# Kernel optimization log

Hardware: AMD Instinct MI355X
Metric: run time of the kernel (lower is better)

The kernel has to match this reference:

```python
import jax, jax.numpy as jnp
import numpy as np

TAU = 2.0      # spikingjelly LIFNode default tau
V_TH = 1.0     # default v_threshold
ALPHA = 4.0    # default surrogate.Sigmoid alpha


@jax.custom_vjp
def spike_fn(v):
    # Heaviside(v - v_th) with sigmoid surrogate gradient
    return (v >= V_TH).astype(v.dtype)

def _spike_fwd(v):
    return (v >= V_TH).astype(v.dtype), v

def _spike_bwd(v, g):
    s = jax.nn.sigmoid(ALPHA * (v - V_TH))
    return (g * ALPHA * s * (1.0 - s),)

spike_fn.defvjp(_spike_fwd, _spike_bwd)


def lif(x):
    """Multi-step LIF: decay_input=False, hard reset to v_reset=0, detach_reset.
    x: [T, B, C, N] -> spikes [T, B, C, N]."""
    def step(v, xt):
        v = v * (1.0 - 1.0 / TAU) + xt          # v = v - (v - 0)/tau + x
        s = spike_fn(v)
        v = v * (1.0 - jax.lax.stop_gradient(s))  # hard reset, detached spike
        return v, s
    v0 = jnp.zeros_like(x[0])
    _, spikes = jax.lax.scan(step, v0, x)
    return spikes


def setup_inputs() -> dict:
    key = jax.random.key(0)
    kx, k1, k2, k3 = jax.random.split(key, 4)
    T, B, C, dim = 4, 32, 196, 768
    scale = dim ** -0.5
    x = jax.random.normal(kx, (T, B, C, dim), dtype=jnp.float32)
    w1 = jax.random.normal(k1, (dim, dim), dtype=jnp.float32) * scale
    w2 = jax.random.normal(k2, (dim, dim), dtype=jnp.float32) * scale
    w3 = jax.random.normal(k3, (dim, dim), dtype=jnp.float32) * scale
    return {"x": x, "w1": w1, "w2": w2, "w3": w3}


def reference(x, w1, w2, w3):
    # y1 = mlp1(mlp1_lif(x)); y2 = mlp2(mlp2_lif(x)); out = mlp3(y1 * mlp3_lif(y2))
    y1 = jnp.einsum('tbcn,mn->tbcm', lif(x), w1)
    y2 = jnp.einsum('tbcn,mn->tbcm', lif(x), w2)
    out = jnp.einsum('tbcn,mn->tbcm', y1 * lif(y2), w3)
    return out
```

## Files before the change

### kernel.cpp

```cpp
#include <hip/hip_runtime.h>
#include <stdint.h>

#define T_STEPS 4
#define BC      6272
#define NDIM    768
#define TBC     (T_STEPS*BC)
#define BCN     (BC*NDIM)
#define FIX_CAP 65536

typedef unsigned short u16;
typedef __attribute__((ext_vector_type(8))) __bf16 bf16x8;
typedef __attribute__((ext_vector_type(4))) float f32x4;
typedef __attribute__((ext_vector_type(4))) int   i32x4;

#define MFMA16(a,b,c)  __builtin_amdgcn_mfma_f32_16x16x32_bf16((a),(b),(c),0,0,0)
#define MFMAI8(a,b,c)  __builtin_amdgcn_mfma_i32_16x16x64_i8((a),(b),(c),0,0,0)
#define SBAR()   __builtin_amdgcn_s_barrier()
#define SCHED0() __builtin_amdgcn_sched_barrier(0)

__device__ __forceinline__ u16 f2b(float f) {
    uint32_t u = __builtin_bit_cast(uint32_t, f);
    u += 0x7FFFu + ((u >> 16) & 1u);
    return (u16)(u >> 16);
}
__device__ __forceinline__ void gload16(const void* g, void* l) {
    __builtin_amdgcn_global_load_lds((const __attribute__((address_space(1))) void*)g,
                                     (__attribute__((address_space(3))) void*)l,
                                     16, 0, 0);
}

__global__ __launch_bounds__(256) void front_kernel(
    const float* __restrict__ x,
    const float* __restrict__ w1, const float* __restrict__ w2,
    const float* __restrict__ w3,
    int8_t* __restrict__ s8, u16* __restrict__ cnt,
    int8_t* __restrict__ w1q, int8_t* __restrict__ w2h,
    int8_t* __restrict__ w2l, u16* __restrict__ w3b,
    uint32_t* __restrict__ fix_cnt)
{
    if (blockIdx.x < BC / 4) {
        const int bc   = blockIdx.x * 4 + (threadIdx.x >> 6);
        const int lane = threadIdx.x & 63;
        const size_t base = (size_t)bc * NDIM + lane * 12;

        double v[12];
        #pragma unroll
        for (int j = 0; j < 12; ++j) v[j] = 0.0;
        uint32_t c01 = 0, c23 = 0;

        #pragma unroll
        for (int t = 0; t < T_STEPS; ++t) {
            float4 xa = *(const float4*)&x[(size_t)t * BCN + base + 0];
            float4 xb = *(const float4*)&x[(size_t)t * BCN + base + 4];
            float4 xc = *(const float4*)&x[(size_t)t * BCN + base + 8];
            float xs[12] = {xa.x, xa.y, xa.z, xa.w, xb.x, xb.y, xb.z, xb.w,
                            xc.x, xc.y, xc.z, xc.w};
            uint32_t pk[3] = {0, 0, 0};
            uint32_t csum = 0;
            #pragma unroll
            for (int j = 0; j < 12; ++j) {
                v[j] = 0.5 * v[j] + (double)xs[j];
                if (v[j] >= 1.0) {
                    pk[j >> 2] |= 1u << ((j & 3) * 8);
                    csum++;
                    v[j] = 0.0;
                }
            }
            uint32_t* dst = (uint32_t*)&s8[(size_t)t * BCN + base];
            dst[0] = pk[0]; dst[1] = pk[1]; dst[2] = pk[2];
            if (t < 2) c01 += csum << (t * 16);
            else       c23 += csum << ((t - 2) * 16);
        }
        #pragma unroll
        for (int o = 32; o > 0; o >>= 1) {
            c01 += __shfl_xor(c01, o);
            c23 += __shfl_xor(c23, o);
        }
        if (lane == 0) {
            cnt[0 * BC + bc] = (u16)(c01 & 0xFFFF);
            cnt[1 * BC + bc] = (u16)(c01 >> 16);
            cnt[2 * BC + bc] = (u16)(c23 & 0xFFFF);
            cnt[3 * BC + bc] = (u16)(c23 >> 16);
        }
    } else {
        int i = (blockIdx.x - BC / 4) * 256 + threadIdx.x;
        if (i == 0) *fix_cnt = 0;
        int q1 = __float2int_rn(w1[i] * 512.0f);
        q1 = q1 > 127 ? 127 : (q1 < -127 ? -127 : q1);
        w1q[i] = (int8_t)q1;
        int q16 = __double2int_rn((double)w2[i] * 65536.0);
        int8_t lo = (int8_t)(q16 & 0xFF);
        int hi = (q16 - (int)lo) >> 8;
        w2h[i] = (int8_t)hi;
        w2l[i] = lo;
        w3b[i] = f2b(w3[i]);
    }
}

__global__ __launch_bounds__(256, 2) void y12_kernel(
    const int8_t* __restrict__ s8,
    const int8_t* __restrict__ w1q, const int8_t* __restrict__ w2hb,
    const int8_t* __restrict__ w2lb,
    const u16* __restrict__ cnt,
    u16* __restrict__ z,
    uint32_t* __restrict__ fix_cnt,
    int2* __restrict__ fix_idx, float4* __restrict__ fix_y1)
{
    __shared__ int8_t lds[4][20480];

    const int lane = threadIdx.x & 63;
    const int wid  = threadIdx.x >> 6;

    const int bid = blockIdx.x;
    const int swz = (bid & 7) * 294 + (bid >> 3);
    const int mb  = swz % (NDIM / 64);
    const int rb  = swz / (NDIM / 64);
    const int m0  = mb * 64;
    const int bc0 = rb * 32;

    const int srow  = lane >> 2;
    const int scolB = ((lane & 3) ^ ((lane >> 3) & 3)) << 4;
    const int8_t* gp[5];
    int lofs[5];
    #pragma unroll
    for (int c = 0; c < 5; ++c) {
        int chunk = wid * 5 + c;
        const int8_t* g;
        int l;
        if (chunk < 8) {
            int gr = chunk * 16 + srow;
            int t = gr >> 5, bcl = gr & 31;
            g = s8 + ((size_t)(t * BC + bc0 + bcl)) * NDIM + scolB;
            l = chunk * 1024;
        } else if (chunk < 12) {
            int mr = (chunk - 8) * 16 + srow;
            g = w1q + ((size_t)(m0 + mr)) * NDIM + scolB;
            l = 8192 + (chunk - 8) * 1024;
        } else if (chunk < 16) {
            int mr = (chunk - 12) * 16 + srow;
            g = w2hb + ((size_t)(m0 + mr)) * NDIM + scolB;
            l = 12288 + (chunk - 12) * 1024;
        } else {
            int mr = (chunk - 16) * 16 + srow;
            g = w2lb + ((size_t)(m0 + mr)) * NDIM + scolB;
            l = 16384 + (chunk - 16) * 1024;
        }
        gp[c] = g;
        lofs[c] = l;
    }

    const int slotb = (((lane >> 4) ^ ((lane >> 1) & 3)) << 4);
    int aoff[4][2];
    #pragma unroll
    for (int t = 0; t < 4; ++t)
        #pragma unroll
        for (int rt = 0; rt < 2; ++rt)
            aoff[t][rt] = (t * 32 + rt * 16 + (lane & 15)) * 64 + slotb;
    const int boff = (wid * 16 + (lane & 15)) * 64 + slotb;

    i32x4 a1[4][2], ah[4][2], al[4][2];
    #pragma unroll
    for (int t = 0; t < 4; ++t)
        #pragma unroll
        for (int rt = 0; rt < 2; ++rt) {
            a1[t][rt] = (i32x4){0, 0, 0, 0};
            ah[t][rt] = (i32x4){0, 0, 0, 0};
            al[t][rt] = (i32x4){0, 0, 0, 0};
        }

    auto stage = [&](int buf) {
        #pragma unroll
        for (int c = 0; c < 5; ++c) {
            gload16(gp[c], &lds[buf][lofs[c]]);
            gp[c] += 64;
        }
    };
    auto compute = [&](int buf) {
        const int8_t* L = lds[buf];
        i32x4 b1 = *(const i32x4*)&L[ 8192 + boff];
        i32x4 bh = *(const i32x4*)&L[12288 + boff];
        i32x4 bl = *(const i32x4*)&L[16384 + boff];
        #pragma unroll
        for (int t = 0; t < 4; ++t)
            #pragma unroll
            for (int rt = 0; rt < 2; ++rt) {
                i32x4 a = *(const i32x4*)&L[aoff[t][rt]];
                a1[t][rt] = MFMAI8(a, b1, a1[t][rt]);
                ah[t][rt] = MFMAI8(a, bh, ah[t][rt]);
                al[t][rt] = MFMAI8(a, bl, al[t][rt]);
            }
    };

    stage(0); stage(1); stage(2);
    for (int t = 0; t < 9; ++t) {
        stage((t + 3) & 3);
        SCHED0();
        asm volatile("s_waitcnt vmcnt(15)" ::: "memory");
        SBAR();
        SCHED0();
        __builtin_amdgcn_s_setprio(1);
        compute(t & 3);
        __builtin_amdgcn_s_setprio(0);
        SCHED0();
        SBAR();
    }
    asm volatile("s_waitcnt vmcnt(10)" ::: "memory");
    SBAR(); SCHED0();
    __builtin_amdgcn_s_setprio(1); compute(1); __builtin_amdgcn_s_setprio(0);
    SCHED0(); SBAR();
    asm volatile("s_waitcnt vmcnt(5)" ::: "memory");
    SBAR(); SCHED0();
    __builtin_amdgcn_s_setprio(1); compute(2); __builtin_amdgcn_s_setprio(0);
    SCHED0(); SBAR();
    asm volatile("s_waitcnt vmcnt(0)" ::: "memory");
    SBAR(); SCHED0();
    __builtin_amdgcn_s_setprio(1); compute(3); __builtin_amdgcn_s_setprio(0);

    const int mg = m0 + wid * 16 + (lane & 15);
    #pragma unroll
    for (int rt = 0; rt < 2; ++rt) {
        #pragma unroll
        for (int r = 0; r < 4; ++r) {
            const int bcg = bc0 + rt * 16 + (lane >> 4) * 4 + r;
            double v = 0.0, e = 0.0;
            bool flag = false;
            float zv[4], y1v[4];
            #pragma unroll
            for (int t = 0; t < 4; ++t) {
                float y1 = (float)a1[t][rt][r] * (1.0f / 512.0f);
                y1v[t] = y1;
                double y2 = (double)(ah[t][rt][r] * 256 + al[t][rt][r])
                            * (1.0 / 65536.0);
                v = 0.5 * v + y2;
                e = 0.5 * e + 7.62939453125e-6 * (double)cnt[t * BC + bcg] + 1e-9;
                double d = v - 1.0;
                flag |= (d <= e && d >= -e);
                if (v >= 1.0) { zv[t] = y1; v = 0.0; e = 0.0; }
                else          { zv[t] = 0.0f; }
            }
            if (flag) {
                uint32_t id = atomicAdd(fix_cnt, 1u);
                if (id < FIX_CAP) {
                    fix_idx[id] = make_int2(bcg, mg);
                    fix_y1[id]  = make_float4(y1v[0], y1v[1], y1v[2], y1v[3]);
                }
            }
            #pragma unroll
            for (int t = 0; t < 4; ++t)
                z[((size_t)(t * BC + bcg)) * NDIM + mg] = f2b(zv[t]);
        }
    }
}

__global__ __launch_bounds__(256) void fixup_kernel(
    const int8_t* __restrict__ s8, const float* __restrict__ w2,
    const int2* __restrict__ fix_idx, const float4* __restrict__ fix_y1,
    const uint32_t* __restrict__ fix_cnt, u16* __restrict__ z)
{
    const int lane = threadIdx.x & 63;
    const int wave = (blockIdx.x * 256 + threadIdx.x) >> 6;
    const int nw   = gridDim.x * 4;
    uint32_t n = *fix_cnt;
    if (n > FIX_CAP) n = FIX_CAP;

    for (uint32_t e = wave; e < n; e += nw) {
        const int bc = fix_idx[e].x, m = fix_idx[e].y;
        const float* w2row = w2 + (size_t)m * NDIM;
        double acc[4] = {0.0, 0.0, 0.0, 0.0};
        #pragma unroll
        for (int j = 0; j < NDIM / 64; ++j) {
            int nn = lane + j * 64;
            double wv = (double)w2row[nn];
            #pragma unroll
            for (int t = 0; t < 4; ++t)
                if (s8[((size_t)(t * BC + bc)) * NDIM + nn]) acc[t] += wv;
        }
        #pragma unroll
        for (int o = 32; o > 0; o >>= 1)
            #pragma unroll
            for (int t = 0; t < 4; ++t) acc[t] += __shfl_xor(acc[t], o);
        if (lane == 0) {
            float4 y1 = fix_y1[e];
            float y1a[4] = {y1.x, y1.y, y1.z, y1.w};
            double v = 0.0;
            #pragma unroll
            for (int t = 0; t < 4; ++t) {
                v = 0.5 * v + acc[t];
                u16 zz = 0;
                if (v >= 1.0) { zz = f2b(y1a[t]); v = 0.0; }
                z[((size_t)(t * BC + bc)) * NDIM + m] = zz;
            }
        }
    }
}

__global__ __launch_bounds__(256, 2) void out_kernel(
    const u16* __restrict__ z, const u16* __restrict__ w3b,
    float* __restrict__ out)
{
    __shared__ u16 lds[2][16384];

    const int lane = threadIdx.x & 63;
    const int wid  = threadIdx.x >> 6;
    const int rw   = wid >> 1;
    const int cw   = wid & 1;

    const int bid = blockIdx.x;
    const int swz = (bid & 7) * 147 + (bid >> 3);
    const int mb  = swz % (NDIM / 128);
    const int rb  = swz / (NDIM / 128);
    const int m0  = mb * 128;
    const int r0  = rb * 128;

    const int srow  = lane >> 3;
    const int scolE = ((((lane & 7) << 4) ^ ((srow & 7) << 4)) >> 1);
    const u16* gp[8];
    int lofs[8];
    #pragma unroll
    for (int c = 0; c < 8; ++c) {
        int chunk = wid * 8 + c;
        const u16* g;
        if (chunk < 16) {
            int gr = chunk * 8 + srow;
            g = z + ((size_t)(r0 + gr)) * NDIM + scolE;
        } else {
            int mr = (chunk - 16) * 8 + srow;
            g = w3b + ((size_t)(m0 + mr)) * NDIM + scolE;
        }
        gp[c] = g;
        lofs[c] = chunk * 512;
    }

    const int swzb = (lane & 7) << 4;
    const int cb   = (lane >> 4) << 4;
    const int colE0 = ((cb     ) ^ swzb) >> 1;
    const int colE1 = ((cb | 64) ^ swzb) >> 1;

    f32x4 acc[4][4];
    #pragma unroll
    for (int rt = 0; rt < 4; ++rt)
        #pragma unroll
        for (int cf = 0; cf < 4; ++cf) acc[rt][cf] = (f32x4){0.f, 0.f, 0.f, 0.f};

    auto stage = [&](int buf) {
        #pragma unroll
        for (int c = 0; c < 8; ++c) {
            gload16(gp[c], &lds[buf][lofs[c]]);
            gp[c] += 64;
        }
    };
    auto compute = [&](int buf) {
        const u16* L = lds[buf];
        #pragma unroll
        for (int k2i = 0; k2i < 2; ++k2i) {
            const int ce = k2i ? colE1 : colE0;
            bf16x8 bw[4];
            #pragma unroll
            for (int cf = 0; cf < 4; ++cf)
                bw[cf] = *(const bf16x8*)&L[8192 + (cw * 64 + cf * 16 + (lane & 15)) * 64 + ce];
            #pragma unroll
            for (int rt = 0; rt < 4; ++rt) {
                bf16x8 az = *(const bf16x8*)&L[(rw * 64 + rt * 16 + (lane & 15)) * 64 + ce];
                #pragma unroll
                for (int cf = 0; cf < 4; ++cf)
                    acc[rt][cf] = MFMA16(az, bw[cf], acc[rt][cf]);
            }
        }
    };

    stage(0);
    __syncthreads();
    for (int it = 0; it < 11; ++it) {
        stage((it + 1) & 1);
        compute(it & 1);
        __syncthreads();
    }
    compute(1);

    #pragma unroll
    for (int rt = 0; rt < 4; ++rt)
        #pragma unroll
        for (int cf = 0; cf < 4; ++cf)
            #pragma unroll
            for (int r = 0; r < 4; ++r)
                out[((size_t)(r0 + rw * 64 + rt * 16 + (lane >> 4) * 4 + r)) * NDIM
                    + m0 + cw * 64 + cf * 16 + (lane & 15)] = acc[rt][cf][r];
}

extern "C" void kernel_launch(void* const* d_in, const int* in_sizes, int n_in,
                              void* d_out, int out_size, void* d_ws, size_t ws_size,
                              hipStream_t stream) {
    const float* x  = (const float*)d_in[0];
    const float* w1 = (const float*)d_in[1];
    const float* w2 = (const float*)d_in[2];
    const float* w3 = (const float*)d_in[3];
    float* out = (float*)d_out;

    char* ws = (char*)d_ws;
    int8_t*   s8      = (int8_t*)(ws);
    u16*      z       = (u16*)(ws + 19267584);
    int8_t*   w1q     = (int8_t*)(ws + 57802752);
    int8_t*   w2h     = (int8_t*)(ws + 58392576);
    int8_t*   w2l     = (int8_t*)(ws + 58982400);
    u16*      w3b     = (u16*)(ws + 59572224);
    u16*      cnt     = (u16*)(ws + 60751872);
    uint32_t* fix_cnt = (uint32_t*)(ws + 60802048);
    int2*     fix_idx = (int2*)(ws + 60802112);
    float4*   fix_y1  = (float4*)(ws + 61326400);

    front_kernel<<<BC / 4 + (NDIM * NDIM) / 256, 256, 0, stream>>>(
        x, w1, w2, w3, s8, cnt, w1q, w2h, w2l, w3b, fix_cnt);
    y12_kernel<<<(BC / 32) * (NDIM / 64), 256, 0, stream>>>(s8, w1q, w2h, w2l,
                                                            cnt, z, fix_cnt,
                                                            fix_idx, fix_y1);
    fixup_kernel<<<128, 256, 0, stream>>>(s8, w2, fix_idx, fix_y1, fix_cnt, z);
    out_kernel<<<(TBC / 128) * (NDIM / 128), 256, 0, stream>>>(z, w3b, out);
}
```

Baseline: 133.3 us.

## Switch y12 GEMM to double-buffered LDS with higher occupancy target

```diff
diff --git a/kernel.cpp b/kernel.cpp
--- a/kernel.cpp
+++ b/kernel.cpp
@@ -15,8 +15,6 @@
 
 #define MFMA16(a,b,c)  __builtin_amdgcn_mfma_f32_16x16x32_bf16((a),(b),(c),0,0,0)
 #define MFMAI8(a,b,c)  __builtin_amdgcn_mfma_i32_16x16x64_i8((a),(b),(c),0,0,0)
-#define SBAR()   __builtin_amdgcn_s_barrier()
-#define SCHED0() __builtin_amdgcn_sched_barrier(0)
 
 __device__ __forceinline__ u16 f2b(float f) {
     uint32_t u = __builtin_bit_cast(uint32_t, f);
@@ -97,7 +95,7 @@
     }
 }
 
-__global__ __launch_bounds__(256, 2) void y12_kernel(
+__global__ __launch_bounds__(256, 4) void y12_kernel(
     const int8_t* __restrict__ s8,
     const int8_t* __restrict__ w1q, const int8_t* __restrict__ w2hb,
     const int8_t* __restrict__ w2lb,
@@ -106,7 +104,7 @@
     uint32_t* __restrict__ fix_cnt,
     int2* __restrict__ fix_idx, float4* __restrict__ fix_y1)
 {
-    __shared__ int8_t lds[4][20480];
+    __shared__ int8_t lds[2][20480];
 
     const int lane = threadIdx.x & 63;
     const int wid  = threadIdx.x >> 6;
@@ -191,30 +189,14 @@
             }
     };
 
-    stage(0); stage(1); stage(2);
-    for (int t = 0; t < 9; ++t) {
-        stage((t + 3) & 3);
-        SCHED0();
-        asm volatile("s_waitcnt vmcnt(15)" ::: "memory");
-        SBAR();
-        SCHED0();
-        __builtin_amdgcn_s_setprio(1);
-        compute(t & 3);
-        __builtin_amdgcn_s_setprio(0);
-        SCHED0();
-        SBAR();
-    }
-    asm volatile("s_waitcnt vmcnt(10)" ::: "memory");
-    SBAR(); SCHED0();
-    __builtin_amdgcn_s_setprio(1); compute(1); __builtin_amdgcn_s_setprio(0);
-    SCHED0(); SBAR();
-    asm volatile("s_waitcnt vmcnt(5)" ::: "memory");
-    SBAR(); SCHED0();
-    __builtin_amdgcn_s_setprio(1); compute(2); __builtin_amdgcn_s_setprio(0);
-    SCHED0(); SBAR();
-    asm volatile("s_waitcnt vmcnt(0)" ::: "memory");
-    SBAR(); SCHED0();
-    __builtin_amdgcn_s_setprio(1); compute(3); __builtin_amdgcn_s_setprio(0);
+    stage(0);
+    __syncthreads();
+    for (int it = 0; it < 11; ++it) {
+        stage((it + 1) & 1);
+        compute(it & 1);
+        __syncthreads();
+    }
+    compute(1);
 
     const int mg = m0 + wid * 16 + (lane & 15);
     #pragma unroll
```

After: 164.8 us. 23.7% more time.
